# Performance work log

Measured on AMD Instinct MI355X. Metric: run time of the kernel, lower is better.

## Reference

```python
import jax, jax.numpy as jnp
import numpy as np

N_NODES = 50000
N_EDGES = 800000
D_IN = 16
H = 128
D_OUT = 8
N_LAYERS = 4


def _init_linear(key, fan_in, fan_out):
    # torch init: weight ~ N(0, 1/sqrt(in_features)), bias = 0
    W = jax.random.normal(key, (fan_in, fan_out), dtype=jnp.float32) / jnp.sqrt(jnp.float32(fan_in))
    b = jnp.zeros((fan_out,), dtype=jnp.float32)
    return W, b


def _mlp2(x, W1, b1, W2, b2):
    # 2-layer MLP: Linear -> GELU(exact) -> Linear
    h = jax.nn.gelu(x @ W1 + b1, approximate=False)
    return h @ W2 + b2


def setup_inputs() -> dict:
    key = jax.random.key(0)
    ks = jax.random.split(key, 16)
    node_features = jax.random.normal(ks[0], (N_NODES, D_IN), dtype=jnp.float32)
    edge_index = jax.random.randint(ks[1], (2, N_EDGES), 0, N_NODES, dtype=jnp.int64 if jax.config.jax_enable_x64 else jnp.int32)
    enc_W1, enc_b1 = _init_linear(ks[2], D_IN, H)
    enc_W2, enc_b2 = _init_linear(ks[3], H, H)
    dec_W1, dec_b1 = _init_linear(ks[4], H, H)
    dec_W2, dec_b2 = _init_linear(ks[5], H, D_OUT)
    # stacked per-layer params for the message-passing blocks
    eW1 = jnp.stack([_init_linear(jax.random.fold_in(ks[6], l), 2 * H, H)[0] for l in range(N_LAYERS)])
    eW2 = jnp.stack([_init_linear(jax.random.fold_in(ks[7], l), H, H)[0] for l in range(N_LAYERS)])
    nW1 = jnp.stack([_init_linear(jax.random.fold_in(ks[8], l), 2 * H, H)[0] for l in range(N_LAYERS)])
    nW2 = jnp.stack([_init_linear(jax.random.fold_in(ks[9], l), H, H)[0] for l in range(N_LAYERS)])
    eb1 = jnp.zeros((N_LAYERS, H), dtype=jnp.float32)
    eb2 = jnp.zeros((N_LAYERS, H), dtype=jnp.float32)
    nb1 = jnp.zeros((N_LAYERS, H), dtype=jnp.float32)
    nb2 = jnp.zeros((N_LAYERS, H), dtype=jnp.float32)
    return dict(node_features=node_features, edge_index=edge_index,
                enc_W1=enc_W1, enc_b1=enc_b1, enc_W2=enc_W2, enc_b2=enc_b2,
                edge_W1=eW1, edge_b1=eb1, edge_W2=eW2, edge_b2=eb2,
                node_W1=nW1, node_b1=nb1, node_W2=nW2, node_b2=nb2,
                dec_W1=dec_W1, dec_b1=dec_b1, dec_W2=dec_W2, dec_b2=dec_b2)


def reference(node_features, edge_index,
              enc_W1, enc_b1, enc_W2, enc_b2,
              edge_W1, edge_b1, edge_W2, edge_b2,
              node_W1, node_b1, node_W2, node_b2,
              dec_W1, dec_b1, dec_W2, dec_b2):
    src = edge_index[0]
    dst = edge_index[1]
    # encode
    h = _mlp2(node_features, enc_W1, enc_b1, enc_W2, enc_b2)  # [N, H]
    # process: residual message-passing blocks with sum aggregation
    for l in range(edge_W1.shape[0]):
        edge_input = jnp.concatenate([h[src], h[dst]], axis=-1)  # [E, 2H]
        message = _mlp2(edge_input, edge_W1[l], edge_b1[l], edge_W2[l], edge_b2[l])  # [E, H]
        aggregated = jax.ops.segment_sum(message, dst, num_segments=h.shape[0])  # [N, H]
        node_update = _mlp2(jnp.concatenate([h, aggregated], axis=-1),
                            node_W1[l], node_b1[l], node_W2[l], node_b2[l])
        h = h + node_update
    # decode
    return _mlp2(h, dec_W1, dec_b1, dec_W2, dec_b2)  # [N, D_OUT]
```

## Files before the change

### kernel.cpp

```cpp
#include <hip/hip_runtime.h>
#include <math.h>


constexpr int H = 128;
constexpr int NTHR = 256;
constexpr int TE = 64;
constexpr int TILE = 32;
constexpr int CHUNK = 16;

using bf16x8 = __attribute__((ext_vector_type(8))) short;
using f32x4  = __attribute__((ext_vector_type(4))) float;

__device__ __forceinline__ float gelu_fast(float x) {
    const float u = fabsf(x) * 0.70710678118654752440f;
    const float t = __builtin_amdgcn_rcpf(fmaf(0.3275911f, u, 1.f));
    float p = fmaf(1.061405429f, t, -1.453152027f);
    p = fmaf(p, t, 1.421413741f);
    p = fmaf(p, t, -0.284496736f);
    p = fmaf(p, t, 0.254829592f);
    p = p * t;
    const float e = __expf(-u * u);
    float er = fmaf(-p, e, 1.f);
    er = copysignf(er, x);
    return 0.5f * x * (1.f + er);
}

__device__ __forceinline__ unsigned short f2bf(float f) {
    unsigned int u = __builtin_bit_cast(unsigned int, f);
    u = (u + 0x7fffu + ((u >> 16) & 1u)) >> 16;
    return (unsigned short)u;
}

__device__ __forceinline__ float bf2f_lo(unsigned int v) {
    return __builtin_bit_cast(float, v << 16);
}
__device__ __forceinline__ float bf2f_hi(unsigned int v) {
    return __builtin_bit_cast(float, v & 0xffff0000u);
}

__global__ __launch_bounds__(NTHR) void prep_kernel(
    const float* __restrict__ eW1, const float* __restrict__ nW2,
    const float* __restrict__ nW1, unsigned short* __restrict__ eW1t,
    unsigned short* __restrict__ nW2t, unsigned short* __restrict__ nW1tc,
    int t1, int t2) {
    const int i = blockIdx.x * NTHR + threadIdx.x;
    if (i < t1) {
        const int per = 2 * H * H;
        const int l = i / per;
        const int r = i - l * per;
        const int n = r % H;
        const int k = r / H;
        eW1t[(size_t)l * per + n * 2 * H + k] = f2bf(eW1[i]);
    } else if (i < t1 + t2) {
        const int j = i - t1;
        const int per = H * H;
        const int l = j / per;
        const int r = j - l * per;
        const int n = r % H;
        const int k = r / H;
        nW2t[(size_t)l * per + n * H + k] = f2bf(nW2[j]);
    } else if (i < t1 + 2 * t2) {
        const int j = i - t1 - t2;
        const int per = H * H;
        const int l = j / per;
        const int r = j - l * per;
        const int k = r / H;
        const int o = r % H;
        nW1tc[(size_t)l * H * 2 * H + o * 2 * H + k] =
            f2bf(nW1[(size_t)l * 2 * H * H + k * H + o]);
    }
}

__global__ __launch_bounds__(H) void wcomb_kernel(
    const float* __restrict__ eW2, const float* __restrict__ eb2,
    const float* __restrict__ nW1, unsigned short* __restrict__ W1tc,
    float* __restrict__ cvec) {
    const int l = blockIdx.y;
    const int j = blockIdx.x;
    const int o = threadIdx.x;
    const float* w1 = nW1 + (size_t)l * 2 * H * H + (size_t)H * H;
    const float* row = (j < H) ? (eW2 + (size_t)l * H * H + (size_t)j * H)
                               : (eb2 + (size_t)l * H);
    float s = 0.f;
#pragma unroll 4
    for (int c = 0; c < H; ++c) s = fmaf(row[c], w1[(size_t)c * H + o], s);
    if (j < H)
        W1tc[(size_t)l * H * 2 * H + o * 2 * H + H + j] = f2bf(s);
    else
        cvec[(size_t)l * H + o] = s;
}

__global__ __launch_bounds__(NTHR) void deg_kernel(const int* __restrict__ dst,
                                                   int* __restrict__ deg, int E) {
    const int e = blockIdx.x * NTHR + threadIdx.x;
    if (e < E) atomicAdd(&deg[dst[e]], 1);
}

__global__ __launch_bounds__(1024) void scan1_kernel(
    const int* __restrict__ deg, int* __restrict__ out,
    int* __restrict__ bsum, int N) {
    __shared__ int buf[1024];
    const int t = threadIdx.x;
    const int i = blockIdx.x * 1024 + t;
    const int x = (i < N) ? deg[i] : 0;
    buf[t] = x;
    __syncthreads();
    int v = x;
    for (int off = 1; off < 1024; off <<= 1) {
        const int y = (t >= off) ? buf[t - off] : 0;
        __syncthreads();
        v += y;
        buf[t] = v;
        __syncthreads();
    }
    if (i < N) out[i] = v - x;
    if (t == 1023) bsum[blockIdx.x] = v;
}

__global__ void scan2_kernel(int* __restrict__ bsum, int nb) {
    if (threadIdx.x == 0) {
        int acc = 0;
        for (int i = 0; i < nb; ++i) {
            const int t = bsum[i];
            bsum[i] = acc;
            acc += t;
        }
    }
}

__global__ __launch_bounds__(NTHR) void scan3_kernel(
    int* __restrict__ out, int* __restrict__ cursor,
    const int* __restrict__ bsum, int N, int E) {
    const int i = blockIdx.x * NTHR + threadIdx.x;
    if (i < N) {
        const int v = out[i] + bsum[i >> 10];
        out[i] = v;
        cursor[i] = v;
    } else if (i == N) {
        out[N] = E;
    }
}

__global__ __launch_bounds__(NTHR) void chunk_kernel(
    const int* __restrict__ rowStart, int* __restrict__ chunkLo, int N) {
    const int n = blockIdx.x * NTHR + threadIdx.x;
    if (n < N) atomicMin(&chunkLo[rowStart[n] / CHUNK], n);
}

__global__ __launch_bounds__(NTHR) void scatter_kernel(
    const int* __restrict__ src, const int* __restrict__ dst,
    int* __restrict__ cursor, int* __restrict__ srcS, int E) {
    const int e = blockIdx.x * NTHR + threadIdx.x;
    if (e >= E) return;
    const int pos = atomicAdd(&cursor[dst[e]], 1);
    srcS[pos] = src[e] << 8;
}

__global__ __launch_bounds__(NTHR) void ab_kernel(
    const unsigned short* __restrict__ h_bf,
    const unsigned short* __restrict__ W1t,
    const float* __restrict__ b1, unsigned short* __restrict__ A,
    float* __restrict__ Bout, int N) {
    __shared__ __align__(16) unsigned short X[TE * H];
    const int t = threadIdx.x;
    const int lane = t & 63;
    const int w = t >> 6;
    const int n0 = blockIdx.x * TE;
    const int l15 = lane & 15;
    const int lq = lane >> 4;

#pragma unroll
    for (int i = 0; i < 4; ++i) {
        const int c = i * NTHR + t;
        const int row = c >> 4;
        const int col8 = c & 15;
        const int n = n0 + row;
        const int4 v = (n < N)
            ? *reinterpret_cast<const int4*>(h_bf + (size_t)n * H + col8 * 8)
            : make_int4(0, 0, 0, 0);
        const int byteoff = row * 256 + ((col8 * 16) ^ ((row & 7) << 4));
        *reinterpret_cast<int4*>(reinterpret_cast<char*>(X) + byteoff) = v;
    }

    const int half = w >> 1;
    const int cbase = (w & 1) * 64;
    bf16x8 Bf[4][4];
#pragma unroll
    for (int cg = 0; cg < 4; ++cg) {
        const int col = cbase + cg * 16 + l15;
#pragma unroll
        for (int s = 0; s < 4; ++s)
            Bf[cg][s] = *reinterpret_cast<const bf16x8*>(
                W1t + (size_t)col * 256 + half * 128 + s * 32 + lq * 8);
    }
    __syncthreads();

    f32x4 acc[4][4];
#pragma unroll
    for (int rg = 0; rg < 4; ++rg)
#pragma unroll
        for (int cg = 0; cg < 4; ++cg) acc[rg][cg] = (f32x4)0.f;

#pragma unroll
    for (int s = 0; s < 4; ++s) {
        bf16x8 a[4];
#pragma unroll
        for (int rg = 0; rg < 4; ++rg) {
            const int row = rg * 16 + l15;
            const int byteoff = row * 256 + ((s * 64 + lq * 16) ^ ((row & 7) << 4));
            a[rg] = *reinterpret_cast<const bf16x8*>(
                reinterpret_cast<const char*>(X) + byteoff);
        }
#pragma unroll
        for (int rg = 0; rg < 4; ++rg)
#pragma unroll
            for (int cg = 0; cg < 4; ++cg)
                acc[rg][cg] = __builtin_amdgcn_mfma_f32_16x16x32_bf16(
                    a[rg], Bf[cg][s], acc[rg][cg], 0, 0, 0);
    }

#pragma unroll
    for (int cg = 0; cg < 4; ++cg) {
        const int col = cbase + cg * 16 + l15;
        const float bb = (half == 1) ? b1[col] : 0.f;
#pragma unroll
        for (int rg = 0; rg < 4; ++rg) {
#pragma unroll
            for (int r = 0; r < 4; ++r) {
                const int row = rg * 16 + lq * 4 + r;
                const int n = n0 + row;
                if (n < N) {
                    if (half == 0)
                        A[(size_t)n * H + col] = f2bf(acc[rg][cg][r]);
                    else
                        Bout[(size_t)n * H + col] = acc[rg][cg][r] + bb;
                }
            }
        }
    }
}

__global__ __launch_bounds__(NTHR) void edge_gather_kernel(
    const unsigned short* __restrict__ A, const float* __restrict__ B,
    const int* __restrict__ srcS, const int* __restrict__ rowStart,
    const int* __restrict__ chunkLo, unsigned short* __restrict__ aggB,
    int N, int E) {
    const int lane = threadIdx.x & 63;
    const int c = blockIdx.x * 4 + (threadIdx.x >> 6);
    const int nWaves = E / CHUNK + 1;
    if (c >= nWaves) return;
    int n = chunkLo[c];
    if (n >= N) return;
    const int Wend = (c + 1) * CHUNK;
    const int c2 = lane * 2;
    const char* Abase = (const char*)A + (size_t)(lane * 4);
    int r0 = rowStart[n];
    while (true) {
        const int r1 = rowStart[n + 1];
        const float2 bv = *reinterpret_cast<const float2*>(B + (size_t)n * H + c2);
        float s0 = 0.f, s1 = 0.f;
        int e = r0;
        for (; e + 4 <= r1; e += 4) {
            const int sa = srcS[e];
            const int sb = srcS[e + 1];
            const int sc = srcS[e + 2];
            const int sd = srcS[e + 3];
            const unsigned int va =
                *reinterpret_cast<const unsigned int*>(Abase + sa);
            const unsigned int vb =
                *reinterpret_cast<const unsigned int*>(Abase + sb);
            const unsigned int vc =
                *reinterpret_cast<const unsigned int*>(Abase + sc);
            const unsigned int vd =
                *reinterpret_cast<const unsigned int*>(Abase + sd);
            s0 += gelu_fast(bf2f_lo(va) + bv.x);
            s1 += gelu_fast(bf2f_hi(va) + bv.y);
            s0 += gelu_fast(bf2f_lo(vb) + bv.x);
            s1 += gelu_fast(bf2f_hi(vb) + bv.y);
            s0 += gelu_fast(bf2f_lo(vc) + bv.x);
            s1 += gelu_fast(bf2f_hi(vc) + bv.y);
            s0 += gelu_fast(bf2f_lo(vd) + bv.x);
            s1 += gelu_fast(bf2f_hi(vd) + bv.y);
        }
        for (; e < r1; ++e) {
            const unsigned int av =
                *reinterpret_cast<const unsigned int*>(Abase + srcS[e]);
            s0 += gelu_fast(bf2f_lo(av) + bv.x);
            s1 += gelu_fast(bf2f_hi(av) + bv.y);
        }
        const unsigned int packed =
            (unsigned int)f2bf(s0) | ((unsigned int)f2bf(s1) << 16);
        *reinterpret_cast<unsigned int*>(aggB + (size_t)n * H + c2) = packed;
        if (++n >= N) break;
        r0 = r1;
        if (r0 >= Wend) break;
    }
}

template <bool PROD>
__global__ __launch_bounds__(NTHR) void node_fused_kernel(
    float* __restrict__ h, unsigned short* __restrict__ h_bf,
    const unsigned short* __restrict__ aggB, const int* __restrict__ deg,
    const unsigned short* __restrict__ W1tc, const float* __restrict__ b1,
    const float* __restrict__ cvec, const unsigned short* __restrict__ W2t,
    const float* __restrict__ b2, const unsigned short* __restrict__ eW1tN,
    const float* __restrict__ eb1N, unsigned short* __restrict__ A_out,
    float* __restrict__ B_out, int N) {
    __shared__ __align__(16) unsigned short X[TE * 256];
    __shared__ int degS[TE];
    const int t = threadIdx.x;
    const int lane = t & 63;
    const int w = t >> 6;
    const int n0 = blockIdx.x * TE;
    const int l15 = lane & 15;
    const int lq = lane >> 4;

    if (t < TE) degS[t] = (n0 + t < N) ? deg[n0 + t] : 0;
#pragma unroll
    for (int i = 0; i < 8; ++i) {
        const int c = i * NTHR + t;
        const int row = c >> 5;
        const int col8 = c & 31;
        const int n = n0 + row;
        int4 v = make_int4(0, 0, 0, 0);
        if (n < N) {
            const unsigned short* srcp = (col8 < 16) ? h_bf : aggB;
            v = *reinterpret_cast<const int4*>(srcp + (size_t)n * H +
                                               (col8 & 15) * 8);
        }
        const int byteoff = row * 512 + ((col8 * 16) ^ ((row & 7) << 4));
        *reinterpret_cast<int4*>(reinterpret_cast<char*>(X) + byteoff) = v;
    }

    bf16x8 B1[2][8];
#pragma unroll
    for (int cg = 0; cg < 2; ++cg) {
        const int col = w * 32 + cg * 16 + l15;
#pragma unroll
        for (int s = 0; s < 8; ++s)
            B1[cg][s] = *reinterpret_cast<const bf16x8*>(
                W1tc + (size_t)col * 256 + s * 32 + lq * 8);
    }
    __syncthreads();

    f32x4 acc[4][2];
#pragma unroll
    for (int rg = 0; rg < 4; ++rg)
#pragma unroll
        for (int cg = 0; cg < 2; ++cg) acc[rg][cg] = (f32x4)0.f;

#pragma unroll
    for (int s = 0; s < 8; ++s) {
        bf16x8 a[4];
#pragma unroll
        for (int rg = 0; rg < 4; ++rg) {
            const int row = rg * 16 + l15;
            const int byteoff = row * 512 + ((s * 64 + lq * 16) ^ ((row & 7) << 4));
            a[rg] = *reinterpret_cast<const bf16x8*>(
                reinterpret_cast<const char*>(X) + byteoff);
        }
#pragma unroll
        for (int rg = 0; rg < 4; ++rg)
#pragma unroll
            for (int cg = 0; cg < 2; ++cg)
                acc[rg][cg] = __builtin_amdgcn_mfma_f32_16x16x32_bf16(
                    a[rg], B1[cg][s], acc[rg][cg], 0, 0, 0);
    }
    __syncthreads();

#pragma unroll
    for (int cg = 0; cg < 2; ++cg) {
        const int col = w * 32 + cg * 16 + l15;
        const float bb = b1[col];
        const float cc = cvec[col];
#pragma unroll
        for (int rg = 0; rg < 4; ++rg) {
#pragma unroll
            for (int r = 0; r < 4; ++r) {
                const int row = rg * 16 + lq * 4 + r;
                const float v =
                    gelu_fast(acc[rg][cg][r] + bb + (float)degS[row] * cc);
                const int byteoff = row * 256 + ((col * 2) ^ ((row & 7) << 4));
                *reinterpret_cast<unsigned short*>(
                    reinterpret_cast<char*>(X) + byteoff) = f2bf(v);
            }
        }
    }

    bf16x8 B2[2][4];
#pragma unroll
    for (int cg = 0; cg < 2; ++cg) {
        const int col = w * 32 + cg * 16 + l15;
#pragma unroll
        for (int s = 0; s < 4; ++s)
            B2[cg][s] = *reinterpret_cast<const bf16x8*>(
                W2t + (size_t)col * 128 + s * 32 + lq * 8);
    }
    __syncthreads();

    f32x4 acc2[4][2];
#pragma unroll
    for (int rg = 0; rg < 4; ++rg)
#pragma unroll
        for (int cg = 0; cg < 2; ++cg) acc2[rg][cg] = (f32x4)0.f;

#pragma unroll
    for (int s = 0; s < 4; ++s) {
        bf16x8 a[4];
#pragma unroll
        for (int rg = 0; rg < 4; ++rg) {
            const int row = rg * 16 + l15;
            const int byteoff = row * 256 + ((s * 64 + lq * 16) ^ ((row & 7) << 4));
            a[rg] = *reinterpret_cast<const bf16x8*>(
                reinterpret_cast<const char*>(X) + byteoff);
        }
#pragma unroll
        for (int rg = 0; rg < 4; ++rg)
#pragma unroll
            for (int cg = 0; cg < 2; ++cg)
                acc2[rg][cg] = __builtin_amdgcn_mfma_f32_16x16x32_bf16(
                    a[rg], B2[cg][s], acc2[rg][cg], 0, 0, 0);
    }

#pragma unroll
    for (int cg = 0; cg < 2; ++cg) {
        const int col = w * 32 + cg * 16 + l15;
        const float bb = b2[col];
#pragma unroll
        for (int rg = 0; rg < 4; ++rg) {
#pragma unroll
            for (int r = 0; r < 4; ++r) {
                const int row = rg * 16 + lq * 4 + r;
                const int n = n0 + row;
                if (n < N) {
                    const float hv = h[(size_t)n * H + col] + acc2[rg][cg][r] + bb;
                    h[(size_t)n * H + col] = hv;
                    const unsigned short hb = f2bf(hv);
                    h_bf[(size_t)n * H + col] = hb;
                    if (PROD) {
                        const int byteoff =
                            16384 + row * 256 + ((col * 2) ^ ((row & 7) << 4));
                        *reinterpret_cast<unsigned short*>(
                            reinterpret_cast<char*>(X) + byteoff) = hb;
                    }
                } else if (PROD) {
                    const int byteoff =
                        16384 + row * 256 + ((col * 2) ^ ((row & 7) << 4));
                    *reinterpret_cast<unsigned short*>(
                        reinterpret_cast<char*>(X) + byteoff) = 0;
                }
            }
        }
    }

    if (PROD) {
        bf16x8 B3[2][4], B4[2][4];
#pragma unroll
        for (int cg = 0; cg < 2; ++cg) {
            const int col = w * 32 + cg * 16 + l15;
#pragma unroll
            for (int s = 0; s < 4; ++s) {
                B3[cg][s] = *reinterpret_cast<const bf16x8*>(
                    eW1tN + (size_t)col * 256 + s * 32 + lq * 8);
                B4[cg][s] = *reinterpret_cast<const bf16x8*>(
                    eW1tN + (size_t)col * 256 + 128 + s * 32 + lq * 8);
            }
        }
        __syncthreads();

        f32x4 acc3[4][2], acc4[4][2];
#pragma unroll
        for (int rg = 0; rg < 4; ++rg)
#pragma unroll
            for (int cg = 0; cg < 2; ++cg) {
                acc3[rg][cg] = (f32x4)0.f;
                acc4[rg][cg] = (f32x4)0.f;
            }

#pragma unroll
        for (int s = 0; s < 4; ++s) {
            bf16x8 a[4];
#pragma unroll
            for (int rg = 0; rg < 4; ++rg) {
                const int row = rg * 16 + l15;
                const int byteoff =
                    16384 + row * 256 + ((s * 64 + lq * 16) ^ ((row & 7) << 4));
                a[rg] = *reinterpret_cast<const bf16x8*>(
                    reinterpret_cast<const char*>(X) + byteoff);
            }
#pragma unroll
            for (int rg = 0; rg < 4; ++rg)
#pragma unroll
                for (int cg = 0; cg < 2; ++cg) {
                    acc3[rg][cg] = __builtin_amdgcn_mfma_f32_16x16x32_bf16(
                        a[rg], B3[cg][s], acc3[rg][cg], 0, 0, 0);
                    acc4[rg][cg] = __builtin_amdgcn_mfma_f32_16x16x32_bf16(
                        a[rg], B4[cg][s], acc4[rg][cg], 0, 0, 0);
                }
        }

#pragma unroll
        for (int cg = 0; cg < 2; ++cg) {
            const int col = w * 32 + cg * 16 + l15;
            const float bb = eb1N[col];
#pragma unroll
            for (int rg = 0; rg < 4; ++rg) {
#pragma unroll
                for (int r = 0; r < 4; ++r) {
                    const int row = rg * 16 + lq * 4 + r;
                    const int n = n0 + row;
                    if (n < N) {
                        A_out[(size_t)n * H + col] = f2bf(acc3[rg][cg][r]);
                        B_out[(size_t)n * H + col] = acc4[rg][cg][r] + bb;
                    }
                }
            }
        }
    }
}

template <int K4>
__device__ __forceinline__ void mlp_layer(const float* __restrict__ W,
                                          const float* lds, int ldsStride,
                                          int c0, int egBase,
                                          float a0[8], float a1[8]) {
#pragma unroll 2
    for (int k4 = 0; k4 < K4; ++k4) {
        const float w00 = W[(k4 * 4 + 0) * H + c0];
        const float w01 = W[(k4 * 4 + 1) * H + c0];
        const float w02 = W[(k4 * 4 + 2) * H + c0];
        const float w03 = W[(k4 * 4 + 3) * H + c0];
        const float w10 = W[(k4 * 4 + 0) * H + c0 + 64];
        const float w11 = W[(k4 * 4 + 1) * H + c0 + 64];
        const float w12 = W[(k4 * 4 + 2) * H + c0 + 64];
        const float w13 = W[(k4 * 4 + 3) * H + c0 + 64];
#pragma unroll
        for (int e = 0; e < 8; ++e) {
            const float4 x = *reinterpret_cast<const float4*>(
                &lds[(egBase + e) * ldsStride + k4 * 4]);
            a0[e] = fmaf(x.x, w00, a0[e]);
            a0[e] = fmaf(x.y, w01, a0[e]);
            a0[e] = fmaf(x.z, w02, a0[e]);
            a0[e] = fmaf(x.w, w03, a0[e]);
            a1[e] = fmaf(x.x, w10, a1[e]);
            a1[e] = fmaf(x.y, w11, a1[e]);
            a1[e] = fmaf(x.z, w12, a1[e]);
            a1[e] = fmaf(x.w, w13, a1[e]);
        }
    }
}

__global__ __launch_bounds__(NTHR) void encode_kernel(
    const float* __restrict__ nf, const float* __restrict__ W1,
    const float* __restrict__ b1, const float* __restrict__ W2,
    const float* __restrict__ b2, float* __restrict__ h,
    unsigned short* __restrict__ h_bf, int N) {
    __shared__ float xin[TILE * 16];
    __shared__ float hm[TILE * H];
    const int t = threadIdx.x;
    const int n0 = blockIdx.x * TILE;
    const int c0 = t & 63;
    const int eg = t >> 6;

    for (int i = t; i < TILE * 16; i += NTHR) {
        const int gi = n0 * 16 + i;
        xin[i] = (gi < N * 16) ? nf[gi] : 0.f;
    }
    __syncthreads();

    float a0[8], a1[8];
#pragma unroll
    for (int e = 0; e < 8; ++e) { a0[e] = 0.f; a1[e] = 0.f; }
    mlp_layer<4>(W1, xin, 16, c0, eg * 8, a0, a1);
    {
        const float bb0 = b1[c0], bb1 = b1[c0 + 64];
#pragma unroll
        for (int e = 0; e < 8; ++e) {
            hm[(eg * 8 + e) * H + c0] = gelu_fast(a0[e] + bb0);
            hm[(eg * 8 + e) * H + c0 + 64] = gelu_fast(a1[e] + bb1);
        }
    }
    __syncthreads();
#pragma unroll
    for (int e = 0; e < 8; ++e) { a0[e] = 0.f; a1[e] = 0.f; }
    mlp_layer<32>(W2, hm, H, c0, eg * 8, a0, a1);
    const float bb0 = b2[c0], bb1 = b2[c0 + 64];
#pragma unroll
    for (int e = 0; e < 8; ++e) {
        const int n = n0 + eg * 8 + e;
        if (n < N) {
            const float v0 = a0[e] + bb0, v1 = a1[e] + bb1;
            h[(size_t)n * H + c0] = v0;
            h[(size_t)n * H + c0 + 64] = v1;
            h_bf[(size_t)n * H + c0] = f2bf(v0);
            h_bf[(size_t)n * H + c0 + 64] = f2bf(v1);
        }
    }
}

__global__ __launch_bounds__(NTHR) void decode_kernel(
    const float* __restrict__ h, const float* __restrict__ W1,
    const float* __restrict__ b1, const float* __restrict__ W2,
    const float* __restrict__ b2, float* __restrict__ out, int N) {
    __shared__ float xin[TILE * H];
    __shared__ float hm[TILE * 132];
    const int t = threadIdx.x;
    const int n0 = blockIdx.x * TILE;
    const int c0 = t & 63;
    const int eg = t >> 6;
    {
        const int col = t & 127;
        for (int e = t >> 7; e < TILE; e += 2) {
            const int n = n0 + e;
            xin[e * H + col] = (n < N) ? h[(size_t)n * H + col] : 0.f;
        }
    }
    __syncthreads();

    float a0[8], a1[8];
#pragma unroll
    for (int e = 0; e < 8; ++e) { a0[e] = 0.f; a1[e] = 0.f; }
    mlp_layer<32>(W1, xin, H, c0, eg * 8, a0, a1);
    {
        const float bb0 = b1[c0], bb1 = b1[c0 + 64];
#pragma unroll
        for (int e = 0; e < 8; ++e) {
            hm[(eg * 8 + e) * 132 + c0] = gelu_fast(a0[e] + bb0);
            hm[(eg * 8 + e) * 132 + c0 + 64] = gelu_fast(a1[e] + bb1);
        }
    }
    __syncthreads();
    {
        const int e = t >> 3;
        const int o = t & 7;
        const int n = n0 + e;
        float acc = b2[o];
#pragma unroll 4
        for (int k = 0; k < H; ++k)
            acc = fmaf(hm[e * 132 + k], W2[k * 8 + o], acc);
        if (n < N) out[n * 8 + o] = acc;
    }
}

extern "C" void kernel_launch(void* const* d_in, const int* in_sizes, int n_in,
                              void* d_out, int out_size, void* d_ws,
                              size_t ws_size, hipStream_t stream) {
    (void)n_in; (void)out_size; (void)ws_size;
    const float* nf      = (const float*)d_in[0];
    const int*   ei      = (const int*)d_in[1];
    const float* enc_W1  = (const float*)d_in[2];
    const float* enc_b1  = (const float*)d_in[3];
    const float* enc_W2  = (const float*)d_in[4];
    const float* enc_b2  = (const float*)d_in[5];
    const float* edge_W1 = (const float*)d_in[6];
    const float* edge_b1 = (const float*)d_in[7];
    const float* edge_W2 = (const float*)d_in[8];
    const float* edge_b2 = (const float*)d_in[9];
    const float* node_W1 = (const float*)d_in[10];
    const float* node_b1 = (const float*)d_in[11];
    const float* node_W2 = (const float*)d_in[12];
    const float* node_b2 = (const float*)d_in[13];
    const float* dec_W1  = (const float*)d_in[14];
    const float* dec_b1  = (const float*)d_in[15];
    const float* dec_W2  = (const float*)d_in[16];
    const float* dec_b2  = (const float*)d_in[17];

    const int N = in_sizes[0] / 16;
    const int E = in_sizes[1] / 2;
    const int L = in_sizes[7] / H;
    const int numChunks = E / CHUNK + 1;

    char* ws = (char*)d_ws;
    float* h    = (float*)ws;                    ws += (size_t)N * H * 4;
    float* Bf32 = (float*)ws;                    ws += (size_t)N * H * 4;
    unsigned short* h_bf = (unsigned short*)ws;  ws += (size_t)N * H * 2;
    unsigned short* A_bf = (unsigned short*)ws;  ws += (size_t)N * H * 2;
    unsigned short* aggB = (unsigned short*)ws;  ws += (size_t)N * H * 2;
    int* srcS     = (int*)ws;                    ws += (size_t)E * 4;
    int* deg      = (int*)ws;                    ws += (size_t)N * 4;
    int* rowStart = (int*)ws;                    ws += (size_t)(N + 1) * 4;
    int* cursor   = (int*)ws;                    ws += (size_t)N * 4;
    int* bsum     = (int*)ws;                    ws += (size_t)256 * 4;
    int* chunkLo  = (int*)ws;                    ws += (size_t)numChunks * 4;
    unsigned short* eW1t = (unsigned short*)ws;  ws += (size_t)L * 2 * H * H * 2;
    unsigned short* nW1tc = (unsigned short*)ws; ws += (size_t)L * 2 * H * H * 2;
    unsigned short* nW2t = (unsigned short*)ws;  ws += (size_t)L * H * H * 2;
    float* cvec   = (float*)ws;                  ws += (size_t)L * H * 4;

    const int* srcArr = ei;
    const int* dstArr = ei + E;

    {
        const int t1 = L * 2 * H * H, t2 = L * H * H;
        prep_kernel<<<(t1 + 2 * t2 + NTHR - 1) / NTHR, NTHR, 0, stream>>>(
            edge_W1, node_W2, node_W1, eW1t, nW2t, nW1tc, t1, t2);
        wcomb_kernel<<<dim3(H + 1, L), H, 0, stream>>>(edge_W2, edge_b2,
                                                       node_W1, nW1tc, cvec);
    }

    hipMemsetAsync(deg, 0, (size_t)N * 4, stream);
    deg_kernel<<<(E + NTHR - 1) / NTHR, NTHR, 0, stream>>>(dstArr, deg, E);
    const int nScanB = (N + 1023) / 1024;
    scan1_kernel<<<nScanB, 1024, 0, stream>>>(deg, rowStart, bsum, N);
    scan2_kernel<<<1, 64, 0, stream>>>(bsum, nScanB);
    scan3_kernel<<<(N + 1 + NTHR - 1) / NTHR, NTHR, 0, stream>>>(
        rowStart, cursor, bsum, N, E);
    hipMemsetAsync(chunkLo, 0x7f, (size_t)numChunks * 4, stream);
    chunk_kernel<<<(N + NTHR - 1) / NTHR, NTHR, 0, stream>>>(rowStart, chunkLo, N);
    scatter_kernel<<<(E + NTHR - 1) / NTHR, NTHR, 0, stream>>>(srcArr, dstArr,
                                                               cursor, srcS, E);

    const int encBlocks  = (N + TILE - 1) / TILE;
    const int tileBlocks = (N + TE - 1) / TE;
    const int gatherBlks = (numChunks + 3) / 4;

    encode_kernel<<<encBlocks, NTHR, 0, stream>>>(nf, enc_W1, enc_b1, enc_W2,
                                                  enc_b2, h, h_bf, N);
    ab_kernel<<<tileBlocks, NTHR, 0, stream>>>(h_bf, eW1t, edge_b1, A_bf, Bf32,
                                               N);
    for (int l = 0; l < L; ++l) {
        edge_gather_kernel<<<gatherBlks, NTHR, 0, stream>>>(
            A_bf, Bf32, srcS, rowStart, chunkLo, aggB, N, E);
        if (l + 1 < L) {
            node_fused_kernel<true><<<tileBlocks, NTHR, 0, stream>>>(
                h, h_bf, aggB, deg, nW1tc + (size_t)l * 2 * H * H,
                node_b1 + (size_t)l * H, cvec + (size_t)l * H,
                nW2t + (size_t)l * H * H, node_b2 + (size_t)l * H,
                eW1t + (size_t)(l + 1) * 2 * H * H,
                edge_b1 + (size_t)(l + 1) * H, A_bf, Bf32, N);
        } else {
            node_fused_kernel<false><<<tileBlocks, NTHR, 0, stream>>>(
                h, h_bf, aggB, deg, nW1tc + (size_t)l * 2 * H * H,
                node_b1 + (size_t)l * H, cvec + (size_t)l * H,
                nW2t + (size_t)l * H * H, node_b2 + (size_t)l * H, nullptr,
                nullptr, nullptr, nullptr, N);
        }
    }
    decode_kernel<<<encBlocks, NTHR, 0, stream>>>(h, dec_W1, dec_b1, dec_W2,
                                                  dec_b2, (float*)d_out, N);
}
```

Measured before the change: 693.9 us.

## Merge encode, message-passing layers and decode into one cooperative persistent kernel

Result: slower. 1.814 ms (+161.5%).

```diff
diff --git a/kernel.cpp b/kernel.cpp
--- a/kernel.cpp
+++ b/kernel.cpp
@@ -1,5 +1,8 @@
 #include <hip/hip_runtime.h>
+#include <hip/hip_cooperative_groups.h>
 #include <math.h>
+
+namespace cg = cooperative_groups;
 
 
 constexpr int H = 128;
@@ -156,18 +159,111 @@
     srcS[pos] = src[e] << 8;
 }
 
-__global__ __launch_bounds__(NTHR) void ab_kernel(
-    const unsigned short* __restrict__ h_bf,
-    const unsigned short* __restrict__ W1t,
-    const float* __restrict__ b1, unsigned short* __restrict__ A,
-    float* __restrict__ Bout, int N) {
-    __shared__ __align__(16) unsigned short X[TE * H];
+struct MegaArgs {
+    const float* nf;
+    const float* encW1; const float* encb1;
+    const float* encW2; const float* encb2;
+    float* h; unsigned short* h_bf;
+    unsigned short* A_bf; float* Bf32;
+    unsigned short* aggB;
+    const int* srcS; const int* rowStart; const int* chunkLo; const int* deg;
+    const unsigned short* eW1t;
+    const unsigned short* nW1tc;
+    const unsigned short* nW2t;
+    const float* edge_b1;
+    const float* node_b1; const float* node_b2; const float* cvec;
+    const float* decW1; const float* decb1;
+    const float* decW2; const float* decb2;
+    float* out;
+    int N, E, L, numChunks;
+};
+
+template <int K4>
+__device__ __forceinline__ void mlp_layer(const float* W, const float* lds,
+                                          int ldsStride, int c0, int egBase,
+                                          float a0[8], float a1[8]) {
+#pragma unroll 2
+    for (int k4 = 0; k4 < K4; ++k4) {
+        const float w00 = W[(k4 * 4 + 0) * H + c0];
+        const float w01 = W[(k4 * 4 + 1) * H + c0];
+        const float w02 = W[(k4 * 4 + 2) * H + c0];
+        const float w03 = W[(k4 * 4 + 3) * H + c0];
+        const float w10 = W[(k4 * 4 + 0) * H + c0 + 64];
+        const float w11 = W[(k4 * 4 + 1) * H + c0 + 64];
+        const float w12 = W[(k4 * 4 + 2) * H + c0 + 64];
+        const float w13 = W[(k4 * 4 + 3) * H + c0 + 64];
+#pragma unroll
+        for (int e = 0; e < 8; ++e) {
+            const float4 x = *reinterpret_cast<const float4*>(
+                &lds[(egBase + e) * ldsStride + k4 * 4]);
+            a0[e] = fmaf(x.x, w00, a0[e]);
+            a0[e] = fmaf(x.y, w01, a0[e]);
+            a0[e] = fmaf(x.z, w02, a0[e]);
+            a0[e] = fmaf(x.w, w03, a0[e]);
+            a1[e] = fmaf(x.x, w10, a1[e]);
+            a1[e] = fmaf(x.y, w11, a1[e]);
+            a1[e] = fmaf(x.z, w12, a1[e]);
+            a1[e] = fmaf(x.w, w13, a1[e]);
+        }
+    }
+}
+
+__device__ void encode_body(int tile, const MegaArgs& a, char* smem) {
+    float* xin = (float*)smem;
+    float* hm = (float*)(smem + 2048);
+    const int t = threadIdx.x;
+    const int n0 = tile * TILE;
+    const int c0 = t & 63;
+    const int eg = t >> 6;
+    const int N = a.N;
+    __syncthreads();
+    for (int i = t; i < TILE * 16; i += NTHR) {
+        const int gi = n0 * 16 + i;
+        xin[i] = (gi < N * 16) ? a.nf[gi] : 0.f;
+    }
+    __syncthreads();
+
+    float a0[8], a1[8];
+#pragma unroll
+    for (int e = 0; e < 8; ++e) { a0[e] = 0.f; a1[e] = 0.f; }
+    mlp_layer<4>(a.encW1, xin, 16, c0, eg * 8, a0, a1);
+    {
+        const float bb0 = a.encb1[c0], bb1 = a.encb1[c0 + 64];
+#pragma unroll
+        for (int e = 0; e < 8; ++e) {
+            hm[(eg * 8 + e) * H + c0] = gelu_fast(a0[e] + bb0);
+            hm[(eg * 8 + e) * H + c0 + 64] = gelu_fast(a1[e] + bb1);
+        }
+    }
+    __syncthreads();
+#pragma unroll
+    for (int e = 0; e < 8; ++e) { a0[e] = 0.f; a1[e] = 0.f; }
+    mlp_layer<32>(a.encW2, hm, H, c0, eg * 8, a0, a1);
+    const float bb0 = a.encb2[c0], bb1 = a.encb2[c0 + 64];
+#pragma unroll
+    for (int e = 0; e < 8; ++e) {
+        const int n = n0 + eg * 8 + e;
+        if (n < N) {
+            const float v0 = a0[e] + bb0, v1 = a1[e] + bb1;
+            a.h[(size_t)n * H + c0] = v0;
+            a.h[(size_t)n * H + c0 + 64] = v1;
+            a.h_bf[(size_t)n * H + c0] = f2bf(v0);
+            a.h_bf[(size_t)n * H + c0 + 64] = f2bf(v1);
+        }
+    }
+}
+
+__device__ void ab_body(int tile, const MegaArgs& a, char* smem) {
+    unsigned short* X = (unsigned short*)smem;
     const int t = threadIdx.x;
     const int lane = t & 63;
     const int w = t >> 6;
-    const int n0 = blockIdx.x * TE;
+    const int n0 = tile * TE;
     const int l15 = lane & 15;
     const int lq = lane >> 4;
+    const int N = a.N;
+    const unsigned short* W1t = a.eW1t;
+    __syncthreads();
 
 #pragma unroll
     for (int i = 0; i < 4; ++i) {
@@ -176,7 +272,7 @@
         const int col8 = c & 15;
         const int n = n0 + row;
         const int4 v = (n < N)
-            ? *reinterpret_cast<const int4*>(h_bf + (size_t)n * H + col8 * 8)
+            ? *reinterpret_cast<const int4*>(a.h_bf + (size_t)n * H + col8 * 8)
             : make_int4(0, 0, 0, 0);
         const int byteoff = row * 256 + ((col8 * 16) ^ ((row & 7) << 4));
         *reinterpret_cast<int4*>(reinterpret_cast<char*>(X) + byteoff) = v;
@@ -203,12 +299,12 @@
 
 #pragma unroll
     for (int s = 0; s < 4; ++s) {
-        bf16x8 a[4];
+        bf16x8 av[4];
 #pragma unroll
         for (int rg = 0; rg < 4; ++rg) {
             const int row = rg * 16 + l15;
             const int byteoff = row * 256 + ((s * 64 + lq * 16) ^ ((row & 7) << 4));
-            a[rg] = *reinterpret_cast<const bf16x8*>(
+            av[rg] = *reinterpret_cast<const bf16x8*>(
                 reinterpret_cast<const char*>(X) + byteoff);
         }
 #pragma unroll
@@ -216,13 +312,13 @@
 #pragma unroll
             for (int cg = 0; cg < 4; ++cg)
                 acc[rg][cg] = __builtin_amdgcn_mfma_f32_16x16x32_bf16(
-                    a[rg], Bf[cg][s], acc[rg][cg], 0, 0, 0);
+                    av[rg], Bf[cg][s], acc[rg][cg], 0, 0, 0);
     }
 
 #pragma unroll
     for (int cg = 0; cg < 4; ++cg) {
         const int col = cbase + cg * 16 + l15;
-        const float bb = (half == 1) ? b1[col] : 0.f;
+        const float bb = (half == 1) ? a.edge_b1[col] : 0.f;
 #pragma unroll
         for (int rg = 0; rg < 4; ++rg) {
 #pragma unroll
@@ -231,33 +327,30 @@
                 const int n = n0 + row;
                 if (n < N) {
                     if (half == 0)
-                        A[(size_t)n * H + col] = f2bf(acc[rg][cg][r]);
+                        a.A_bf[(size_t)n * H + col] = f2bf(acc[rg][cg][r]);
                     else
-                        Bout[(size_t)n * H + col] = acc[rg][cg][r] + bb;
+                        a.Bf32[(size_t)n * H + col] = acc[rg][cg][r] + bb;
                 }
             }
         }
     }
 }
 
-__global__ __launch_bounds__(NTHR) void edge_gather_kernel(
-    const unsigned short* __restrict__ A, const float* __restrict__ B,
-    const int* __restrict__ srcS, const int* __restrict__ rowStart,
-    const int* __restrict__ chunkLo, unsigned short* __restrict__ aggB,
-    int N, int E) {
+__device__ void gather_chunk(int c, const MegaArgs& a) {
     const int lane = threadIdx.x & 63;
-    const int c = blockIdx.x * 4 + (threadIdx.x >> 6);
-    const int nWaves = E / CHUNK + 1;
-    if (c >= nWaves) return;
-    int n = chunkLo[c];
+    const int N = a.N;
+    int n = a.chunkLo[c];
     if (n >= N) return;
     const int Wend = (c + 1) * CHUNK;
     const int c2 = lane * 2;
-    const char* Abase = (const char*)A + (size_t)(lane * 4);
+    const char* Abase = (const char*)a.A_bf + (size_t)(lane * 4);
+    const int* srcS = a.srcS;
+    const int* rowStart = a.rowStart;
     int r0 = rowStart[n];
     while (true) {
         const int r1 = rowStart[n + 1];
-        const float2 bv = *reinterpret_cast<const float2*>(B + (size_t)n * H + c2);
+        const float2 bv =
+            *reinterpret_cast<const float2*>(a.Bf32 + (size_t)n * H + c2);
         float s0 = 0.f, s1 = 0.f;
         int e = r0;
         for (; e + 4 <= r1; e += 4) {
@@ -290,32 +383,34 @@
         }
         const unsigned int packed =
             (unsigned int)f2bf(s0) | ((unsigned int)f2bf(s1) << 16);
-        *reinterpret_cast<unsigned int*>(aggB + (size_t)n * H + c2) = packed;
+        *reinterpret_cast<unsigned int*>(a.aggB + (size_t)n * H + c2) = packed;
         if (++n >= N) break;
         r0 = r1;
         if (r0 >= Wend) break;
     }
 }
 
-template <bool PROD>
-__global__ __launch_bounds__(NTHR) void node_fused_kernel(
-    float* __restrict__ h, unsigned short* __restrict__ h_bf,
-    const unsigned short* __restrict__ aggB, const int* __restrict__ deg,
-    const unsigned short* __restrict__ W1tc, const float* __restrict__ b1,
-    const float* __restrict__ cvec, const unsigned short* __restrict__ W2t,
-    const float* __restrict__ b2, const unsigned short* __restrict__ eW1tN,
-    const float* __restrict__ eb1N, unsigned short* __restrict__ A_out,
-    float* __restrict__ B_out, int N) {
-    __shared__ __align__(16) unsigned short X[TE * 256];
-    __shared__ int degS[TE];
+__device__ void node_body(int tile, int l, bool prod, const MegaArgs& a,
+                          char* smem) {
+    unsigned short* X = (unsigned short*)smem;
+    int* degS = (int*)(smem + 32768);
     const int t = threadIdx.x;
     const int lane = t & 63;
     const int w = t >> 6;
-    const int n0 = blockIdx.x * TE;
+    const int n0 = tile * TE;
     const int l15 = lane & 15;
     const int lq = lane >> 4;
-
-    if (t < TE) degS[t] = (n0 + t < N) ? deg[n0 + t] : 0;
+    const int N = a.N;
+    const unsigned short* W1tc = a.nW1tc + (size_t)l * 2 * H * H;
+    const unsigned short* W2t = a.nW2t + (size_t)l * H * H;
+    const float* b1 = a.node_b1 + (size_t)l * H;
+    const float* b2 = a.node_b2 + (size_t)l * H;
+    const float* cvec = a.cvec + (size_t)l * H;
+    const unsigned short* eW1tN = a.eW1t + (size_t)(l + 1) * 2 * H * H;
+    const float* eb1N = a.edge_b1 + (size_t)(l + 1) * H;
+    __syncthreads();
+
+    if (t < TE) degS[t] = (n0 + t < N) ? a.deg[n0 + t] : 0;
 #pragma unroll
     for (int i = 0; i < 8; ++i) {
         const int c = i * NTHR + t;
@@ -324,7 +419,7 @@
         const int n = n0 + row;
         int4 v = make_int4(0, 0, 0, 0);
         if (n < N) {
-            const unsigned short* srcp = (col8 < 16) ? h_bf : aggB;
+            const unsigned short* srcp = (col8 < 16) ? a.h_bf : a.aggB;
             v = *reinterpret_cast<const int4*>(srcp + (size_t)n * H +
                                                (col8 & 15) * 8);
         }
@@ -351,12 +446,12 @@
 
 #pragma unroll
     for (int s = 0; s < 8; ++s) {
-        bf16x8 a[4];
+        bf16x8 av[4];
 #pragma unroll
         for (int rg = 0; rg < 4; ++rg) {
             const int row = rg * 16 + l15;
             const int byteoff = row * 512 + ((s * 64 + lq * 16) ^ ((row & 7) << 4));
-            a[rg] = *reinterpret_cast<const bf16x8*>(
+            av[rg] = *reinterpret_cast<const bf16x8*>(
                 reinterpret_cast<const char*>(X) + byteoff);
         }
 #pragma unroll
@@ -364,7 +459,7 @@
 #pragma unroll
             for (int cg = 0; cg < 2; ++cg)
                 acc[rg][cg] = __builtin_amdgcn_mfma_f32_16x16x32_bf16(
-                    a[rg], B1[cg][s], acc[rg][cg], 0, 0, 0);
+                    av[rg], B1[cg][s], acc[rg][cg], 0, 0, 0);
     }
     __syncthreads();
 
@@ -406,12 +501,12 @@
 
 #pragma unroll
     for (int s = 0; s < 4; ++s) {
-        bf16x8 a[4];
+        bf16x8 av[4];
 #pragma unroll
         for (int rg = 0; rg < 4; ++rg) {
             const int row = rg * 16 + l15;
             const int byteoff = row * 256 + ((s * 64 + lq * 16) ^ ((row & 7) << 4));
-            a[rg] = *reinterpret_cast<const bf16x8*>(
+            av[rg] = *reinterpret_cast<const bf16x8*>(
                 reinterpret_cast<const char*>(X) + byteoff);
         }
 #pragma unroll
@@ -419,7 +514,7 @@
 #pragma unroll
             for (int cg = 0; cg < 2; ++cg)
                 acc2[rg][cg] = __builtin_amdgcn_mfma_f32_16x16x32_bf16(
-                    a[rg], B2[cg][s], acc2[rg][cg], 0, 0, 0);
+                    av[rg], B2[cg][s], acc2[rg][cg], 0, 0, 0);
     }
 
 #pragma unroll
@@ -433,17 +528,18 @@
                 const int row = rg * 16 + lq * 4 + r;
                 const int n = n0 + row;
                 if (n < N) {
-                    const float hv = h[(size_t)n * H + col] + acc2[rg][cg][r] + bb;
-                    h[(size_t)n * H + col] = hv;
+                    const float hv =
+                        a.h[(size_t)n * H + col] + acc2[rg][cg][r] + bb;
+                    a.h[(size_t)n * H + col] = hv;
                     const unsigned short hb = f2bf(hv);
-                    h_bf[(size_t)n * H + col] = hb;
-                    if (PROD) {
+                    a.h_bf[(size_t)n * H + col] = hb;
+                    if (prod) {
                         const int byteoff =
                             16384 + row * 256 + ((col * 2) ^ ((row & 7) << 4));
                         *reinterpret_cast<unsigned short*>(
                             reinterpret_cast<char*>(X) + byteoff) = hb;
                     }
-                } else if (PROD) {
+                } else if (prod) {
                     const int byteoff =
                         16384 + row * 256 + ((col * 2) ^ ((row & 7) << 4));
                     *reinterpret_cast<unsigned short*>(
@@ -453,7 +549,7 @@
         }
     }
 
-    if (PROD) {
+    if (prod) {
         bf16x8 B3[2][4], B4[2][4];
 #pragma unroll
         for (int cg = 0; cg < 2; ++cg) {
@@ -479,13 +575,13 @@
 
 #pragma unroll
         for (int s = 0; s < 4; ++s) {
-            bf16x8 a[4];
+            bf16x8 av[4];
 #pragma unroll
             for (int rg = 0; rg < 4; ++rg) {
                 const int row = rg * 16 + l15;
                 const int byteoff =
                     16384 + row * 256 + ((s * 64 + lq * 16) ^ ((row & 7) << 4));
-                a[rg] = *reinterpret_cast<const bf16x8*>(
+                av[rg] = *reinterpret_cast<const bf16x8*>(
                     reinterpret_cast<const char*>(X) + byteoff);
             }
 #pragma unroll
@@ -493,9 +589,9 @@
 #pragma unroll
                 for (int cg = 0; cg < 2; ++cg) {
                     acc3[rg][cg] = __builtin_amdgcn_mfma_f32_16x16x32_bf16(
-                        a[rg], B3[cg][s], acc3[rg][cg], 0, 0, 0);
+                        av[rg], B3[cg][s], acc3[rg][cg], 0, 0, 0);
                     acc4[rg][cg] = __builtin_amdgcn_mfma_f32_16x16x32_bf16(
-                        a[rg], B4[cg][s], acc4[rg][cg], 0, 0, 0);
+                        av[rg], B4[cg][s], acc4[rg][cg], 0, 0, 0);
                 }
         }
 
@@ -510,8 +606,8 @@
                     const int row = rg * 16 + lq * 4 + r;
                     const int n = n0 + row;
                     if (n < N) {
-                        A_out[(size_t)n * H + col] = f2bf(acc3[rg][cg][r]);
-                        B_out[(size_t)n * H + col] = acc4[rg][cg][r] + bb;
+                        a.A_bf[(size_t)n * H + col] = f2bf(acc3[rg][cg][r]);
+                        a.Bf32[(size_t)n * H + col] = acc4[rg][cg][r] + bb;
                     }
                 }
             }
@@ -519,100 +615,20 @@
     }
 }
 
-template <int K4>
-__device__ __forceinline__ void mlp_layer(const float* __restrict__ W,
-                                          const float* lds, int ldsStride,
-                                          int c0, int egBase,
-                                          float a0[8], float a1[8]) {
-#pragma unroll 2
-    for (int k4 = 0; k4 < K4; ++k4) {
-        const float w00 = W[(k4 * 4 + 0) * H + c0];
-        const float w01 = W[(k4 * 4 + 1) * H + c0];
-        const float w02 = W[(k4 * 4 + 2) * H + c0];
-        const float w03 = W[(k4 * 4 + 3) * H + c0];
-        const float w10 = W[(k4 * 4 + 0) * H + c0 + 64];
-        const float w11 = W[(k4 * 4 + 1) * H + c0 + 64];
-        const float w12 = W[(k4 * 4 + 2) * H + c0 + 64];
-        const float w13 = W[(k4 * 4 + 3) * H + c0 + 64];
-#pragma unroll
-        for (int e = 0; e < 8; ++e) {
-            const float4 x = *reinterpret_cast<const float4*>(
-                &lds[(egBase + e) * ldsStride + k4 * 4]);
-            a0[e] = fmaf(x.x, w00, a0[e]);
-            a0[e] = fmaf(x.y, w01, a0[e]);
-            a0[e] = fmaf(x.z, w02, a0[e]);
-            a0[e] = fmaf(x.w, w03, a0[e]);
-            a1[e] = fmaf(x.x, w10, a1[e]);
-            a1[e] = fmaf(x.y, w11, a1[e]);
-            a1[e] = fmaf(x.z, w12, a1[e]);
-            a1[e] = fmaf(x.w, w13, a1[e]);
-        }
-    }
-}
-
-__global__ __launch_bounds__(NTHR) void encode_kernel(
-    const float* __restrict__ nf, const float* __restrict__ W1,
-    const float* __restrict__ b1, const float* __restrict__ W2,
-    const float* __restrict__ b2, float* __restrict__ h,
-    unsigned short* __restrict__ h_bf, int N) {
-    __shared__ float xin[TILE * 16];
-    __shared__ float hm[TILE * H];
+__device__ void dec_body(int tile, const MegaArgs& a, char* smem) {
+    float* xin = (float*)smem;
+    float* hm = (float*)(smem + 16384);
     const int t = threadIdx.x;
-    const int n0 = blockIdx.x * TILE;
+    const int n0 = tile * TILE;
     const int c0 = t & 63;
     const int eg = t >> 6;
-
-    for (int i = t; i < TILE * 16; i += NTHR) {
-        const int gi = n0 * 16 + i;
-        xin[i] = (gi < N * 16) ? nf[gi] : 0.f;
-    }
-    __syncthreads();
-
-    float a0[8], a1[8];
-#pragma unroll
-    for (int e = 0; e < 8; ++e) { a0[e] = 0.f; a1[e] = 0.f; }
-    mlp_layer<4>(W1, xin, 16, c0, eg * 8, a0, a1);
-    {
-        const float bb0 = b1[c0], bb1 = b1[c0 + 64];
-#pragma unroll
-        for (int e = 0; e < 8; ++e) {
-            hm[(eg * 8 + e) * H + c0] = gelu_fast(a0[e] + bb0);
-            hm[(eg * 8 + e) * H + c0 + 64] = gelu_fast(a1[e] + bb1);
-        }
-    }
-    __syncthreads();
-#pragma unroll
-    for (int e = 0; e < 8; ++e) { a0[e] = 0.f; a1[e] = 0.f; }
-    mlp_layer<32>(W2, hm, H, c0, eg * 8, a0, a1);
-    const float bb0 = b2[c0], bb1 = b2[c0 + 64];
-#pragma unroll
-    for (int e = 0; e < 8; ++e) {
-        const int n = n0 + eg * 8 + e;
-        if (n < N) {
-            const float v0 = a0[e] + bb0, v1 = a1[e] + bb1;
-            h[(size_t)n * H + c0] = v0;
-            h[(size_t)n * H + c0 + 64] = v1;
-            h_bf[(size_t)n * H + c0] = f2bf(v0);
-            h_bf[(size_t)n * H + c0 + 64] = f2bf(v1);
-        }
-    }
-}
-
-__global__ __launch_bounds__(NTHR) void decode_kernel(
-    const float* __restrict__ h, const float* __restrict__ W1,
-    const float* __restrict__ b1, const float* __restrict__ W2,
-    const float* __restrict__ b2, float* __restrict__ out, int N) {
-    __shared__ float xin[TILE * H];
-    __shared__ float hm[TILE * 132];
-    const int t = threadIdx.x;
-    const int n0 = blockIdx.x * TILE;
-    const int c0 = t & 63;
-    const int eg = t >> 6;
+    const int N = a.N;
+    __syncthreads();
     {
         const int col = t & 127;
         for (int e = t >> 7; e < TILE; e += 2) {
             const int n = n0 + e;
-            xin[e * H + col] = (n < N) ? h[(size_t)n * H + col] : 0.f;
+            xin[e * H + col] = (n < N) ? a.h[(size_t)n * H + col] : 0.f;
         }
     }
     __syncthreads();
@@ -620,9 +636,9 @@
     float a0[8], a1[8];
 #pragma unroll
     for (int e = 0; e < 8; ++e) { a0[e] = 0.f; a1[e] = 0.f; }
-    mlp_layer<32>(W1, xin, H, c0, eg * 8, a0, a1);
+    mlp_layer<32>(a.decW1, xin, H, c0, eg * 8, a0, a1);
     {
-        const float bb0 = b1[c0], bb1 = b1[c0 + 64];
+        const float bb0 = a.decb1[c0], bb1 = a.decb1[c0 + 64];
 #pragma unroll
         for (int e = 0; e < 8; ++e) {
             hm[(eg * 8 + e) * 132 + c0] = gelu_fast(a0[e] + bb0);
@@ -634,12 +650,43 @@
         const int e = t >> 3;
         const int o = t & 7;
         const int n = n0 + e;
-        float acc = b2[o];
+        float acc = a.decb2[o];
 #pragma unroll 4
         for (int k = 0; k < H; ++k)
-            acc = fmaf(hm[e * 132 + k], W2[k * 8 + o], acc);
-        if (n < N) out[n * 8 + o] = acc;
-    }
+            acc = fmaf(hm[e * 132 + k], a.decW2[k * 8 + o], acc);
+        if (n < N) a.out[n * 8 + o] = acc;
+    }
+}
+
+__global__ __launch_bounds__(NTHR, 4) void mega_kernel(MegaArgs a) {
+    cg::grid_group grid = cg::this_grid();
+    __shared__ __align__(16) char smem[33792];
+    const int encTiles = (a.N + TILE - 1) / TILE;
+    const int nodeTiles = (a.N + TE - 1) / TE;
+
+    for (int tile = blockIdx.x; tile < encTiles; tile += gridDim.x)
+        encode_body(tile, a, smem);
+    grid.sync();
+
+    for (int tile = blockIdx.x; tile < nodeTiles; tile += gridDim.x)
+        ab_body(tile, a, smem);
+    grid.sync();
+
+    for (int l = 0; l < a.L; ++l) {
+        const int totW = gridDim.x * 4;
+        for (int c = blockIdx.x * 4 + (threadIdx.x >> 6); c < a.numChunks;
+             c += totW)
+            gather_chunk(c, a);
+        grid.sync();
+
+        const bool prod = (l + 1 < a.L);
+        for (int tile = blockIdx.x; tile < nodeTiles; tile += gridDim.x)
+            node_body(tile, l, prod, a, smem);
+        grid.sync();
+    }
+
+    for (int tile = blockIdx.x; tile < encTiles; tile += gridDim.x)
+        dec_body(tile, a, smem);
 }
 
 extern "C" void kernel_launch(void* const* d_in, const int* in_sizes, int n_in,
@@ -710,32 +757,31 @@
     scatter_kernel<<<(E + NTHR - 1) / NTHR, NTHR, 0, stream>>>(srcArr, dstArr,
                                                                cursor, srcS, E);
 
-    const int encBlocks  = (N + TILE - 1) / TILE;
-    const int tileBlocks = (N + TE - 1) / TE;
-    const int gatherBlks = (numChunks + 3) / 4;
-
-    encode_kernel<<<encBlocks, NTHR, 0, stream>>>(nf, enc_W1, enc_b1, enc_W2,
-                                                  enc_b2, h, h_bf, N);
-    ab_kernel<<<tileBlocks, NTHR, 0, stream>>>(h_bf, eW1t, edge_b1, A_bf, Bf32,
-                                               N);
-    for (int l = 0; l < L; ++l) {
-        edge_gather_kernel<<<gatherBlks, NTHR, 0, stream>>>(
-            A_bf, Bf32, srcS, rowStart, chunkLo, aggB, N, E);
-        if (l + 1 < L) {
-            node_fused_kernel<true><<<tileBlocks, NTHR, 0, stream>>>(
-                h, h_bf, aggB, deg, nW1tc + (size_t)l * 2 * H * H,
-                node_b1 + (size_t)l * H, cvec + (size_t)l * H,
-                nW2t + (size_t)l * H * H, node_b2 + (size_t)l * H,
-                eW1t + (size_t)(l + 1) * 2 * H * H,
-                edge_b1 + (size_t)(l + 1) * H, A_bf, Bf32, N);
-        } else {
-            node_fused_kernel<false><<<tileBlocks, NTHR, 0, stream>>>(
-                h, h_bf, aggB, deg, nW1tc + (size_t)l * 2 * H * H,
-                node_b1 + (size_t)l * H, cvec + (size_t)l * H,
-                nW2t + (size_t)l * H * H, node_b2 + (size_t)l * H, nullptr,
-                nullptr, nullptr, nullptr, N);
-        }
-    }
-    decode_kernel<<<encBlocks, NTHR, 0, stream>>>(h, dec_W1, dec_b1, dec_W2,
-                                                  dec_b2, (float*)d_out, N);
-}
+    MegaArgs margs;
+    margs.nf = nf;
+    margs.encW1 = enc_W1; margs.encb1 = enc_b1;
+    margs.encW2 = enc_W2; margs.encb2 = enc_b2;
+    margs.h = h; margs.h_bf = h_bf;
+    margs.A_bf = A_bf; margs.Bf32 = Bf32;
+    margs.aggB = aggB;
+    margs.srcS = srcS; margs.rowStart = rowStart;
+    margs.chunkLo = chunkLo; margs.deg = deg;
+    margs.eW1t = eW1t; margs.nW1tc = nW1tc; margs.nW2t = nW2t;
+    margs.edge_b1 = edge_b1;
+    margs.node_b1 = node_b1; margs.node_b2 = node_b2; margs.cvec = cvec;
+    margs.decW1 = dec_W1; margs.decb1 = dec_b1;
+    margs.decW2 = dec_W2; margs.decb2 = dec_b2;
+    margs.out = (float*)d_out;
+    margs.N = N; margs.E = E; margs.L = L; margs.numChunks = numChunks;
+
+    int blocksPerCU = 0;
+    hipOccupancyMaxActiveBlocksPerMultiprocessor(&blocksPerCU, mega_kernel,
+                                                 NTHR, 0);
+    if (blocksPerCU < 1) blocksPerCU = 1;
+    if (blocksPerCU > 8) blocksPerCU = 8;
+    const int grid = blocksPerCU * 256;
+
+    void* kargs[] = {(void*)&margs};
+    hipLaunchCooperativeKernel((const void*)mega_kernel, dim3(grid),
+                               dim3(NTHR), kargs, 0, stream);
+}
```

## Split edge gather into half-column jobs and fuse graph preprocessing kernels

Applied to the files above, without the earlier changes.

Result: slower. 728.1 us (+4.9%).

```diff
diff --git a/kernel.cpp b/kernel.cpp
--- a/kernel.cpp
+++ b/kernel.cpp
@@ -31,11 +31,8 @@
     return (unsigned short)u;
 }
 
-__device__ __forceinline__ float bf2f_lo(unsigned int v) {
-    return __builtin_bit_cast(float, v << 16);
-}
-__device__ __forceinline__ float bf2f_hi(unsigned int v) {
-    return __builtin_bit_cast(float, v & 0xffff0000u);
+__device__ __forceinline__ float bf2f(unsigned short v) {
+    return __builtin_bit_cast(float, (unsigned int)v << 16);
 }
 
 __global__ __launch_bounds__(NTHR) void prep_kernel(
@@ -130,7 +127,8 @@
 
 __global__ __launch_bounds__(NTHR) void scan3_kernel(
     int* __restrict__ out, int* __restrict__ cursor,
-    const int* __restrict__ bsum, int N, int E) {
+    const int* __restrict__ bsum, int* __restrict__ chunkLo, int N, int E,
+    int numChunks) {
     const int i = blockIdx.x * NTHR + threadIdx.x;
     if (i < N) {
         const int v = out[i] + bsum[i >> 10];
@@ -139,21 +137,19 @@
     } else if (i == N) {
         out[N] = E;
     }
-}
-
-__global__ __launch_bounds__(NTHR) void chunk_kernel(
-    const int* __restrict__ rowStart, int* __restrict__ chunkLo, int N) {
-    const int n = blockIdx.x * NTHR + threadIdx.x;
-    if (n < N) atomicMin(&chunkLo[rowStart[n] / CHUNK], n);
-}
-
-__global__ __launch_bounds__(NTHR) void scatter_kernel(
+    if (i < numChunks) chunkLo[i] = 0x7fffffff;
+}
+
+__global__ __launch_bounds__(NTHR) void finalize_kernel(
+    const int* __restrict__ rowStart, int* __restrict__ chunkLo,
     const int* __restrict__ src, const int* __restrict__ dst,
-    int* __restrict__ cursor, int* __restrict__ srcS, int E) {
-    const int e = blockIdx.x * NTHR + threadIdx.x;
-    if (e >= E) return;
-    const int pos = atomicAdd(&cursor[dst[e]], 1);
-    srcS[pos] = src[e] << 8;
+    int* __restrict__ cursor, int* __restrict__ srcS, int N, int E) {
+    const int i = blockIdx.x * NTHR + threadIdx.x;
+    if (i < N) atomicMin(&chunkLo[rowStart[i] / CHUNK], i);
+    if (i < E) {
+        const int pos = atomicAdd(&cursor[dst[i]], 1);
+        srcS[pos] = src[i] << 8;
+    }
 }
 
 __global__ __launch_bounds__(NTHR) void ab_kernel(
@@ -246,51 +242,54 @@
     const int* __restrict__ chunkLo, unsigned short* __restrict__ aggB,
     int N, int E) {
     const int lane = threadIdx.x & 63;
-    const int c = blockIdx.x * 4 + (threadIdx.x >> 6);
-    const int nWaves = E / CHUNK + 1;
-    if (c >= nWaves) return;
+    const int job = blockIdx.x * 4 + (threadIdx.x >> 6);
+    const int nJobs = (E / CHUNK + 1) * 2;
+    if (job >= nJobs) return;
+    const int c = job >> 1;
+    const int col = (job & 1) * 64 + lane;
     int n = chunkLo[c];
     if (n >= N) return;
     const int Wend = (c + 1) * CHUNK;
-    const int c2 = lane * 2;
-    const char* Abase = (const char*)A + (size_t)(lane * 4);
+    const char* Abase = (const char*)A + (size_t)(col * 2);
     int r0 = rowStart[n];
     while (true) {
         const int r1 = rowStart[n + 1];
-        const float2 bv = *reinterpret_cast<const float2*>(B + (size_t)n * H + c2);
-        float s0 = 0.f, s1 = 0.f;
+        const float bv = B[(size_t)n * H + col];
+        float s = 0.f;
         int e = r0;
+        for (; e + 8 <= r1; e += 8) {
+            unsigned short v0 = *reinterpret_cast<const unsigned short*>(Abase + srcS[e]);
+            unsigned short v1 = *reinterpret_cast<const unsigned short*>(Abase + srcS[e + 1]);
+            unsigned short v2 = *reinterpret_cast<const unsigned short*>(Abase + srcS[e + 2]);
+            unsigned short v3 = *reinterpret_cast<const unsigned short*>(Abase + srcS[e + 3]);
+            unsigned short v4 = *reinterpret_cast<const unsigned short*>(Abase + srcS[e + 4]);
+            unsigned short v5 = *reinterpret_cast<const unsigned short*>(Abase + srcS[e + 5]);
+            unsigned short v6 = *reinterpret_cast<const unsigned short*>(Abase + srcS[e + 6]);
+            unsigned short v7 = *reinterpret_cast<const unsigned short*>(Abase + srcS[e + 7]);
+            s += gelu_fast(bf2f(v0) + bv);
+            s += gelu_fast(bf2f(v1) + bv);
+            s += gelu_fast(bf2f(v2) + bv);
+            s += gelu_fast(bf2f(v3) + bv);
+            s += gelu_fast(bf2f(v4) + bv);
+            s += gelu_fast(bf2f(v5) + bv);
+            s += gelu_fast(bf2f(v6) + bv);
+            s += gelu_fast(bf2f(v7) + bv);
+        }
         for (; e + 4 <= r1; e += 4) {
-            const int sa = srcS[e];
-            const int sb = srcS[e + 1];
-            const int sc = srcS[e + 2];
-            const int sd = srcS[e + 3];
-            const unsigned int va =
-                *reinterpret_cast<const unsigned int*>(Abase + sa);
-            const unsigned int vb =
-                *reinterpret_cast<const unsigned int*>(Abase + sb);
-            const unsigned int vc =
-                *reinterpret_cast<const unsigned int*>(Abase + sc);
-            const unsigned int vd =
-                *reinterpret_cast<const unsigned int*>(Abase + sd);
-            s0 += gelu_fast(bf2f_lo(va) + bv.x);
-            s1 += gelu_fast(bf2f_hi(va) + bv.y);
-            s0 += gelu_fast(bf2f_lo(vb) + bv.x);
-            s1 += gelu_fast(bf2f_hi(vb) + bv.y);
-            s0 += gelu_fast(bf2f_lo(vc) + bv.x);
-            s1 += gelu_fast(bf2f_hi(vc) + bv.y);
-            s0 += gelu_fast(bf2f_lo(vd) + bv.x);
-            s1 += gelu_fast(bf2f_hi(vd) + bv.y);
+            unsigned short v0 = *reinterpret_cast<const unsigned short*>(Abase + srcS[e]);
+            unsigned short v1 = *reinterpret_cast<const unsigned short*>(Abase + srcS[e + 1]);
+            unsigned short v2 = *reinterpret_cast<const unsigned short*>(Abase + srcS[e + 2]);
+            unsigned short v3 = *reinterpret_cast<const unsigned short*>(Abase + srcS[e + 3]);
+            s += gelu_fast(bf2f(v0) + bv);
+            s += gelu_fast(bf2f(v1) + bv);
+            s += gelu_fast(bf2f(v2) + bv);
+            s += gelu_fast(bf2f(v3) + bv);
         }
         for (; e < r1; ++e) {
-            const unsigned int av =
-                *reinterpret_cast<const unsigned int*>(Abase + srcS[e]);
-            s0 += gelu_fast(bf2f_lo(av) + bv.x);
-            s1 += gelu_fast(bf2f_hi(av) + bv.y);
-        }
-        const unsigned int packed =
-            (unsigned int)f2bf(s0) | ((unsigned int)f2bf(s1) << 16);
-        *reinterpret_cast<unsigned int*>(aggB + (size_t)n * H + c2) = packed;
+            unsigned short v0 = *reinterpret_cast<const unsigned short*>(Abase + srcS[e]);
+            s += gelu_fast(bf2f(v0) + bv);
+        }
+        aggB[(size_t)n * H + col] = f2bf(s);
         if (++n >= N) break;
         r0 = r1;
         if (r0 >= Wend) break;
@@ -703,16 +702,16 @@
     const int nScanB = (N + 1023) / 1024;
     scan1_kernel<<<nScanB, 1024, 0, stream>>>(deg, rowStart, bsum, N);
     scan2_kernel<<<1, 64, 0, stream>>>(bsum, nScanB);
-    scan3_kernel<<<(N + 1 + NTHR - 1) / NTHR, NTHR, 0, stream>>>(
-        rowStart, cursor, bsum, N, E);
-    hipMemsetAsync(chunkLo, 0x7f, (size_t)numChunks * 4, stream);
-    chunk_kernel<<<(N + NTHR - 1) / NTHR, NTHR, 0, stream>>>(rowStart, chunkLo, N);
-    scatter_kernel<<<(E + NTHR - 1) / NTHR, NTHR, 0, stream>>>(srcArr, dstArr,
-                                                               cursor, srcS, E);
+    const int scan3Span = (N + 1 > numChunks) ? (N + 1) : numChunks;
+    scan3_kernel<<<(scan3Span + NTHR - 1) / NTHR, NTHR, 0, stream>>>(
+        rowStart, cursor, bsum, chunkLo, N, E, numChunks);
+    const int finSpan = (N > E) ? N : E;
+    finalize_kernel<<<(finSpan + NTHR - 1) / NTHR, NTHR, 0, stream>>>(
+        rowStart, chunkLo, srcArr, dstArr, cursor, srcS, N, E);
 
     const int encBlocks  = (N + TILE - 1) / TILE;
     const int tileBlocks = (N + TE - 1) / TE;
-    const int gatherBlks = (numChunks + 3) / 4;
+    const int gatherBlks = (numChunks * 2 + 3) / 4;
 
     encode_kernel<<<encBlocks, NTHR, 0, stream>>>(nf, enc_W1, enc_b1, enc_W2,
                                                   enc_b2, h, h_bf, N);
```
